# Performance work log

Hardware: AMD Instinct MI355X
Metric: run time of the kernel (lower is better)

Reference implementation:

```python
import jax, jax.numpy as jnp
import numpy as np

B, L, D = 4, 2048, 768
H, K = 12, 9
IPG = D // H  # in-channels per group = head_size = 64
PAD = (K - 1) // 2


def setup_inputs() -> dict:
    key = jax.random.key(0)
    ks = jax.random.split(key, 8)
    s = lambda k, shape, scale: jax.random.normal(k, shape, dtype=jnp.float32) * scale
    return {
        "query": s(ks[0], (B, L, D), 1.0),
        "dw_w": s(ks[1], (D, 1, K), 0.1),          # depthwise Conv1d weight, no bias
        "pw_w": s(ks[2], (H, IPG, IPG), 0.05),     # grouped 1x1 conv [head, out_pg, in_pg]
        "pw_b": s(ks[3], (D,), 0.02),
        "ak_w": s(ks[4], (H, K, IPG), 0.05),       # conv_attn_kernel grouped 1x1 [head, K, in_pg]
        "ak_b": s(ks[5], (H * K,), 0.02),
        "pt_w": s(ks[6], (D, D), 0.02),            # conv_attn_point Linear weight [out, in]
        "pt_b": s(ks[7], (D,), 0.02),
    }


def _sdconv(query, dw_w, pw_w, pw_b, ak_w, ak_b, pt_w, pt_b):
    b, l, d = query.shape
    # SeparableConv1d: depthwise conv (groups=D, kernel K, padding PAD, no bias)
    x = query.transpose(0, 2, 1)  # [B, D, L]
    dw = jax.lax.conv_general_dilated(
        x, dw_w, window_strides=(1,), padding=[(PAD, PAD)],
        feature_group_count=d, dimension_numbers=("NCH", "OIH", "NCH"))  # [B, D, L]
    # grouped pointwise conv (groups=H, kernel 1)
    dwg = dw.reshape(b, H, IPG, l)
    pw = jnp.einsum("bhil,hoi->bhol", dwg, pw_w).reshape(b, d, l) + pw_b[None, :, None]
    key_conv_attn = pw.transpose(0, 2, 1)  # [B, L, D]
    # stride == 1 path: elementwise gate with query
    conv_attn = key_conv_attn * query  # [B, L, D]
    # conv_attn_kernel: grouped 1x1 conv D -> H*K (per head: IPG -> K)
    ca = conv_attn.reshape(b, l, H, IPG)
    kern = jnp.einsum("blhi,hki->blhk", ca, ak_w) + ak_b.reshape(H, K)  # [B, L, H, K]
    w = jax.nn.softmax(kern, axis=-1)  # softmax over kernel positions
    # conv_attn_point linear on value (= query here)
    v = query @ pt_w.T + pt_b  # [B, L, D]
    # unfold: local windows of size K around each position
    vp = jnp.pad(v, ((0, 0), (PAD, PAD), (0, 0)))
    idx = jnp.arange(l)[:, None] + jnp.arange(K)[None, :]  # [L, K]
    win = vp[:, idx]  # [B, L, K, D]
    winh = win.reshape(b, l, K, H, IPG)
    out = jnp.einsum("blkhd,blhk->blhd", winh, w).reshape(b, l, d)
    return out


def reference(query, dw_w, pw_w, pw_b, ak_w, ak_b, pt_w, pt_b):
    return _sdconv(query, dw_w, pw_w, pw_b, ak_w, ak_b, pt_w, pt_b)
```

## Files before the change

kernel.cpp:

```cpp
#include <hip/hip_runtime.h>
#include <math.h>

#define NB 4
#define NL 2048
#define ND 768
#define NH 12
#define NK 9
#define NIPG 64
#define NPAD 4
#define LT 16
#define NGEMM 768

typedef __attribute__((ext_vector_type(8))) short s16x8;
typedef __attribute__((ext_vector_type(4))) float f32x4;

__device__ __forceinline__ unsigned short f2bf(float f) {
  unsigned int u = __float_as_uint(f);
  unsigned int r = (u + 0x7FFFu + ((u >> 16) & 1u)) >> 16;
  return (unsigned short)r;
}
__device__ __forceinline__ float bf2f(unsigned short s) {
  return __uint_as_float(((unsigned int)s) << 16);
}
__device__ __forceinline__ void gload16(const void* g, void* l) {
  __builtin_amdgcn_global_load_lds((const __attribute__((address_space(1))) void*)g,
                                   (__attribute__((address_space(3))) void*)l,
                                   16, 0, 0);
}

__global__ __launch_bounds__(256) void prep(const float* __restrict__ q,
                                            const float* __restrict__ pt_w,
                                            const float* __restrict__ pw_w,
                                            const float* __restrict__ ak_w,
                                            unsigned short* __restrict__ qb,
                                            unsigned short* __restrict__ ptb,
                                            unsigned short* __restrict__ pwb,
                                            unsigned short* __restrict__ akp) {
  const int t = blockIdx.x * 256 + threadIdx.x;
  for (int i = t; i < NB * NL * ND / 4; i += gridDim.x * 256) {
    float4 f = ((const float4*)q)[i];
    ushort4 o; o.x = f2bf(f.x); o.y = f2bf(f.y); o.z = f2bf(f.z); o.w = f2bf(f.w);
    ((ushort4*)qb)[i] = o;
  }
  if (t < ND * ND / 4) {
    float4 f = ((const float4*)pt_w)[t];
    ushort4 o; o.x = f2bf(f.x); o.y = f2bf(f.y); o.z = f2bf(f.z); o.w = f2bf(f.w);
    ((ushort4*)ptb)[t] = o;
  }
  if (t < NH * NIPG * NIPG / 4) {
    float4 f = ((const float4*)pw_w)[t];
    ushort4 o; o.x = f2bf(f.x); o.y = f2bf(f.y); o.z = f2bf(f.z); o.w = f2bf(f.w);
    ((ushort4*)pwb)[t] = o;
  }
  if (t < NH * 16 * NIPG) {
    const int h = t >> 10;
    const int r = t & 1023;
    const int k = r >> 6;
    const int i = r & 63;
    akp[t] = (k < NK) ? f2bf(ak_w[((size_t)h * NK + k) * NIPG + i]) : (unsigned short)0;
  }
}

__global__ __launch_bounds__(256) void fused(const unsigned short* __restrict__ qb,
                                             const unsigned short* __restrict__ ptb,
                                             const float* __restrict__ bias,
                                             unsigned short* __restrict__ v,
                                             const float* __restrict__ dw_w,
                                             const unsigned short* __restrict__ pwb,
                                             const float* __restrict__ pw_b,
                                             const unsigned short* __restrict__ akp,
                                             const float* __restrict__ ak_b,
                                             float* __restrict__ wout) {
  __shared__ unsigned char smem[24576];
  const int t = threadIdx.x;
  const int lane = t & 63;
  const int wv = t >> 6;
  const int fr = lane & 15;
  const int fq = lane >> 4;

  if (blockIdx.x < NGEMM) {
    const int g = blockIdx.x;
    const int xcd = g & 7;
    const int j = g >> 3;
    const long mo = (long)(xcd * 8 + j / 12) * 128;
    const int n0 = (j % 12) * 64;

    const int soff = t * 16;
    const int sr = soff >> 6;
    const int scb = soff & 63;
    const unsigned char* gA0 = (const unsigned char*)qb + (mo + sr) * 1536L + scb;
    const unsigned char* gA1 = gA0 + 64L * 1536;
    const unsigned char* gB  = (const unsigned char*)ptb + (size_t)(n0 + sr) * 1536 + scb;

    int aoff[2], boff[4];
#pragma unroll
    for (int m = 0; m < 2; ++m)
      aoff[m] = ((wv * 32 + m * 16 + fr) * 32 + fq * 8) * 2;
#pragma unroll
    for (int n = 0; n < 4; ++n)
      boff[n] = 8192 + ((n * 16 + fr) * 32 + fq * 8) * 2;

#define STAGE(kt_)                                                 \
    do {                                                           \
      const long kb_ = (long)(kt_) * 64;                           \
      unsigned char* base_ = &smem[((kt_) & 1) * 12288];           \
      gload16(gA0 + kb_, base_ + soff);                            \
      gload16(gA1 + kb_, base_ + 4096 + soff);                     \
      gload16(gB + kb_, base_ + 8192 + soff);                      \
    } while (0)

#define FRAGS(kt_)                                                 \
    do {                                                           \
      const unsigned char* bb_ = &smem[((kt_) & 1) * 12288];       \
      _Pragma("unroll")                                            \
      for (int m_ = 0; m_ < 2; ++m_) av[m_] = *(const s16x8*)&bb_[aoff[m_]]; \
      _Pragma("unroll")                                            \
      for (int n_ = 0; n_ < 4; ++n_) bv[n_] = *(const s16x8*)&bb_[boff[n_]]; \
    } while (0)

#define MM8                                                        \
    do {                                                           \
      _Pragma("unroll")                                            \
      for (int m_ = 0; m_ < 2; ++m_)                               \
        _Pragma("unroll")                                          \
        for (int n_ = 0; n_ < 4; ++n_)                             \
          acc[m_][n_] = __builtin_amdgcn_mfma_f32_16x16x32_bf16(   \
              av[m_], bv[n_], acc[m_][n_], 0, 0, 0);               \
    } while (0)

    f32x4 acc[2][4] = {};
    s16x8 av[2], bv[4];

    STAGE(0);
    STAGE(1);
    for (int kt = 0; kt < 23; ++kt) {
      asm volatile("s_waitcnt vmcnt(3)" ::: "memory");
      __builtin_amdgcn_s_barrier();
      FRAGS(kt);
      asm volatile("s_waitcnt lgkmcnt(0)" ::: "memory");
      __builtin_amdgcn_sched_barrier(0);
      __builtin_amdgcn_s_barrier();
      if (kt + 2 < 24) STAGE(kt + 2);
      MM8;
    }
    {
      asm volatile("s_waitcnt vmcnt(0)" ::: "memory");
      __builtin_amdgcn_s_barrier();
      FRAGS(23);
      MM8;
    }
#undef STAGE
#undef FRAGS
#undef MM8

#pragma unroll
    for (int m = 0; m < 2; ++m) {
#pragma unroll
      for (int n = 0; n < 4; ++n) {
        const long row = mo + wv * 32 + m * 16 + fq * 4;
        const int col = n0 + n * 16 + fr;
        const float bbv = bias[col];
#pragma unroll
        for (int jj = 0; jj < 4; ++jj)
          v[(row + jj) * ND + col] = f2bf(acc[m][n][jj] + bbv);
      }
    }
  } else {
    const int a = blockIdx.x - NGEMM;
    const int l0 = (a & 31) * 64;
    const int h  = (a >> 5) % NH;
    const int b  = a / (32 * NH);
    const int d0 = h * NIPG;

    unsigned short (*qs)[68] = (unsigned short(*)[68])smem;
    unsigned char* ab = smem + 9792;

    const unsigned short* pwh = pwb + (size_t)h * NIPG * NIPG;
    const unsigned short* akh = akp + (size_t)h * 16 * NIPG;
    s16x8 pv0[4], pv1[4];
#pragma unroll
    for (int n = 0; n < 4; ++n) {
      const int o = n * 16 + fr;
      pv0[n] = *(const s16x8*)&pwh[o * 64 + fq * 8];
      pv1[n] = *(const s16x8*)&pwh[o * 64 + 32 + fq * 8];
    }
    s16x8 ak0 = *(const s16x8*)&akh[fr * 64 + fq * 8];
    s16x8 ak1 = *(const s16x8*)&akh[fr * 64 + 32 + fq * 8];
    float dwk[NK];
#pragma unroll
    for (int k = 0; k < NK; ++k) dwk[k] = dw_w[(size_t)(d0 + lane) * NK + k];

    {
      const int sl = t >> 4;
      const int sc = (t & 15) * 4;
      for (int r = sl; r < 72; r += 16) {
        const int l = l0 - NPAD + r;
        ushort4 ub = make_ushort4(0, 0, 0, 0);
        if (l >= 0 && l < NL)
          ub = *(const ushort4*)&qb[((size_t)(b * NL + l)) * ND + d0 + sc];
        *(ushort4*)&qs[r][sc] = ub;
      }
    }
    __syncthreads();

    const int lset = wv * 16;
    {
      float win9[NK];
#pragma unroll
      for (int k = 0; k < NK; ++k) win9[k] = bf2f(qs[lset + k][lane]);
#pragma unroll
      for (int l2 = 0; l2 < 16; ++l2) {
        const int l = lset + l2;
        float s = 0.f;
#pragma unroll
        for (int k = 0; k < NK; ++k) s = fmaf(win9[k], dwk[k], s);
        const int byte = ((l * 64 + lane) * 2) ^ ((l & 7) << 4);
        *(unsigned short*)&ab[byte] = f2bf(s);
        if (l2 < 15) {
#pragma unroll
          for (int k = 0; k < NK - 1; ++k) win9[k] = win9[k + 1];
          win9[NK - 1] = bf2f(qs[lset + l2 + NK][lane]);
        }
      }
    }

    s16x8 av0, av1;
    {
      const int row = lset + fr;
      const int b0 = ((row * 64 + fq * 8) * 2)      ^ ((row & 7) << 4);
      const int b1 = ((row * 64 + 32 + fq * 8) * 2) ^ ((row & 7) << 4);
      av0 = *(const s16x8*)&ab[b0];
      av1 = *(const s16x8*)&ab[b1];
    }
    f32x4 accp[4];
#pragma unroll
    for (int n = 0; n < 4; ++n) {
      accp[n] = (f32x4){0.f, 0.f, 0.f, 0.f};
      accp[n] = __builtin_amdgcn_mfma_f32_16x16x32_bf16(av0, pv0[n], accp[n], 0, 0, 0);
      accp[n] = __builtin_amdgcn_mfma_f32_16x16x32_bf16(av1, pv1[n], accp[n], 0, 0, 0);
    }

#pragma unroll
    for (int n = 0; n < 4; ++n) {
      const int o = n * 16 + fr;
      const float pb = pw_b[d0 + o];
#pragma unroll
      for (int jj = 0; jj < 4; ++jj) {
        const int row = lset + fq * 4 + jj;
        const float ca = (accp[n][jj] + pb) * bf2f(qs[row + NPAD][o]);
        const int byte = ((row * 64 + o) * 2) ^ ((row & 7) << 4);
        *(unsigned short*)&ab[byte] = f2bf(ca);
      }
    }

    f32x4 acck = (f32x4){0.f, 0.f, 0.f, 0.f};
    {
      const int row = lset + fr;
      const int b0 = ((row * 64 + fq * 8) * 2)      ^ ((row & 7) << 4);
      const int b1 = ((row * 64 + 32 + fq * 8) * 2) ^ ((row & 7) << 4);
      s16x8 a0 = *(const s16x8*)&ab[b0];
      s16x8 a1 = *(const s16x8*)&ab[b1];
      acck = __builtin_amdgcn_mfma_f32_16x16x32_bf16(a0, ak0, acck, 0, 0, 0);
      acck = __builtin_amdgcn_mfma_f32_16x16x32_bf16(a1, ak1, acck, 0, 0, 0);
    }

    const bool kvalid = fr < NK;
    const float akbv = kvalid ? ak_b[h * NK + fr] : 0.f;
#pragma unroll
    for (int jj = 0; jj < 4; ++jj) {
      float val = acck[jj] + akbv;
      float mv = kvalid ? val : -3.4e38f;
#pragma unroll
      for (int mm = 1; mm < 16; mm <<= 1) mv = fmaxf(mv, __shfl_xor(mv, mm));
      const float e = kvalid ? __expf(val - mv) : 0.f;
      float ssum = e;
#pragma unroll
      for (int mm = 1; mm < 16; mm <<= 1) ssum += __shfl_xor(ssum, mm);
      if (kvalid) {
        const int row = l0 + lset + fq * 4 + jj;
        wout[(((size_t)(b * NL + row)) * NH + h) * NK + fr] = e / ssum;
      }
    }
  }
}

__global__ __launch_bounds__(192) void sdconv_out(const unsigned short* __restrict__ v,
                                                  const float* __restrict__ w,
                                                  float* __restrict__ out) {
  const int b  = blockIdx.y;
  const int l0 = blockIdx.x * LT;
  const int t  = threadIdx.x;
  const int d  = t * 4;
  const int h  = t >> 4;
  const size_t vbase = (size_t)b * NL * ND + d;

  float4 win[NK];
#pragma unroll
  for (int k = 0; k < NK; ++k) {
    const int r = l0 - NPAD + k;
    if (r >= 0 && r < NL) {
      ushort4 u = *(const ushort4*)&v[vbase + (size_t)r * ND];
      win[k] = make_float4(bf2f(u.x), bf2f(u.y), bf2f(u.z), bf2f(u.w));
    } else {
      win[k] = make_float4(0.f, 0.f, 0.f, 0.f);
    }
  }
#pragma unroll
  for (int l2 = 0; l2 < LT; ++l2) {
    const int l = l0 + l2;
    const float* wp = &w[(((size_t)(b * NL + l)) * NH + h) * NK];
    float4 acc = make_float4(0.f, 0.f, 0.f, 0.f);
#pragma unroll
    for (int k = 0; k < NK; ++k) {
      const float wk = wp[k];
      acc.x = fmaf(wk, win[k].x, acc.x);
      acc.y = fmaf(wk, win[k].y, acc.y);
      acc.z = fmaf(wk, win[k].z, acc.z);
      acc.w = fmaf(wk, win[k].w, acc.w);
    }
    *(float4*)&out[(size_t)(b * NL + l) * ND + d] = acc;
#pragma unroll
    for (int k = 0; k < NK - 1; ++k) win[k] = win[k + 1];
    const int rn = l + NPAD + 1;
    if (rn < NL) {
      ushort4 u = *(const ushort4*)&v[vbase + (size_t)rn * ND];
      win[NK - 1] = make_float4(bf2f(u.x), bf2f(u.y), bf2f(u.z), bf2f(u.w));
    } else {
      win[NK - 1] = make_float4(0.f, 0.f, 0.f, 0.f);
    }
  }
}

extern "C" void kernel_launch(void* const* d_in, const int* in_sizes, int n_in,
                              void* d_out, int out_size, void* d_ws, size_t ws_size,
                              hipStream_t stream) {
  const float* query = (const float*)d_in[0];
  const float* dw_w  = (const float*)d_in[1];
  const float* pw_w  = (const float*)d_in[2];
  const float* pw_b  = (const float*)d_in[3];
  const float* ak_w  = (const float*)d_in[4];
  const float* ak_b  = (const float*)d_in[5];
  const float* pt_w  = (const float*)d_in[6];
  const float* pt_b  = (const float*)d_in[7];
  float* out = (float*)d_out;

  float* w = (float*)d_ws;
  unsigned short* qb  = (unsigned short*)(w + (size_t)NB * NL * NH * NK);
  unsigned short* ptb = qb + (size_t)NB * NL * ND;
  unsigned short* pwb = ptb + (size_t)ND * ND;
  unsigned short* akp = pwb + (size_t)NH * NIPG * NIPG;
  unsigned short* v   = akp + (size_t)NH * 16 * NIPG;

  prep<<<2048, 256, 0, stream>>>(query, pt_w, pw_w, ak_w, qb, ptb, pwb, akp);

  fused<<<NGEMM + 32 * NH * NB, 256, 0, stream>>>(qb, ptb, pt_b, v,
                                                  dw_w, pwb, pw_b, akp, ak_b, w);

  dim3 g3(NL / LT, NB, 1);
  sdconv_out<<<g3, 192, 0, stream>>>(v, w, out);
}
```

Baseline: 138.6 us.

## Enlarge GEMM tiles to 128x128 and process two tiles per attention block

The projection GEMM moves from 128x64 to 128x128 output tiles with a 2x2 wave layout, so each wave computes 64x64 and fetched fragments get more reuse. This halves the GEMM block count and raises LDS use to 32KB. The attention-weight branch now handles two consecutive 64-row tiles per block, amortising the per-block weight loads, at the cost of an extra barrier and half as many blocks. Together these cut total blocks and redundant loads but raise register pressure and may lower occupancy.

```diff
diff --git a/kernel.cpp b/kernel.cpp
--- a/kernel.cpp
+++ b/kernel.cpp
@@ -9,7 +9,7 @@
 #define NIPG 64
 #define NPAD 4
 #define LT 16
-#define NGEMM 768
+#define NGEMM 384
 
 typedef __attribute__((ext_vector_type(8))) short s16x8;
 typedef __attribute__((ext_vector_type(4))) float f32x4;
@@ -71,7 +71,7 @@
                                              const unsigned short* __restrict__ akp,
                                              const float* __restrict__ ak_b,
                                              float* __restrict__ wout) {
-  __shared__ unsigned char smem[24576];
+  __shared__ unsigned char smem[32768];
   const int t = threadIdx.x;
   const int lane = t & 63;
   const int wv = t >> 6;
@@ -82,83 +82,86 @@
     const int g = blockIdx.x;
     const int xcd = g & 7;
     const int j = g >> 3;
-    const long mo = (long)(xcd * 8 + j / 12) * 128;
-    const int n0 = (j % 12) * 64;
+    const long mo = (long)(xcd * 8 + j / 6) * 128;
+    const int n0 = (j % 6) * 128;
+    const int wr = wv >> 1, wc = wv & 1;
 
     const int soff = t * 16;
     const int sr = soff >> 6;
     const int scb = soff & 63;
     const unsigned char* gA0 = (const unsigned char*)qb + (mo + sr) * 1536L + scb;
     const unsigned char* gA1 = gA0 + 64L * 1536;
-    const unsigned char* gB  = (const unsigned char*)ptb + (size_t)(n0 + sr) * 1536 + scb;
-
-    int aoff[2], boff[4];
-#pragma unroll
-    for (int m = 0; m < 2; ++m)
-      aoff[m] = ((wv * 32 + m * 16 + fr) * 32 + fq * 8) * 2;
+    const unsigned char* gB0 = (const unsigned char*)ptb + (size_t)(n0 + sr) * 1536 + scb;
+    const unsigned char* gB1 = gB0 + 64L * 1536;
+
+    int aoff[4], boff[4];
+#pragma unroll
+    for (int m = 0; m < 4; ++m)
+      aoff[m] = ((wr * 64 + m * 16 + fr) * 32 + fq * 8) * 2;
 #pragma unroll
     for (int n = 0; n < 4; ++n)
-      boff[n] = 8192 + ((n * 16 + fr) * 32 + fq * 8) * 2;
+      boff[n] = 8192 + ((wc * 64 + n * 16 + fr) * 32 + fq * 8) * 2;
 
 #define STAGE(kt_)                                                 \
     do {                                                           \
       const long kb_ = (long)(kt_) * 64;                           \
-      unsigned char* base_ = &smem[((kt_) & 1) * 12288];           \
+      unsigned char* base_ = &smem[((kt_) & 1) * 16384];           \
       gload16(gA0 + kb_, base_ + soff);                            \
       gload16(gA1 + kb_, base_ + 4096 + soff);                     \
-      gload16(gB + kb_, base_ + 8192 + soff);                      \
+      gload16(gB0 + kb_, base_ + 8192 + soff);                     \
+      gload16(gB1 + kb_, base_ + 12288 + soff);                    \
     } while (0)
 
 #define FRAGS(kt_)                                                 \
     do {                                                           \
-      const unsigned char* bb_ = &smem[((kt_) & 1) * 12288];       \
+      const unsigned char* bb_ = &smem[((kt_) & 1) * 16384];       \
       _Pragma("unroll")                                            \
-      for (int m_ = 0; m_ < 2; ++m_) av[m_] = *(const s16x8*)&bb_[aoff[m_]]; \
+      for (int m_ = 0; m_ < 4; ++m_) av[m_] = *(const s16x8*)&bb_[aoff[m_]]; \
       _Pragma("unroll")                                            \
       for (int n_ = 0; n_ < 4; ++n_) bv[n_] = *(const s16x8*)&bb_[boff[n_]]; \
     } while (0)
 
-#define MM8                                                        \
+#define MM16                                                       \
     do {                                                           \
       _Pragma("unroll")                                            \
-      for (int m_ = 0; m_ < 2; ++m_)                               \
+      for (int m_ = 0; m_ < 4; ++m_)                               \
         _Pragma("unroll")                                          \
         for (int n_ = 0; n_ < 4; ++n_)                             \
           acc[m_][n_] = __builtin_amdgcn_mfma_f32_16x16x32_bf16(   \
               av[m_], bv[n_], acc[m_][n_], 0, 0, 0);               \
     } while (0)
 
-    f32x4 acc[2][4] = {};
-    s16x8 av[2], bv[4];
+    f32x4 acc[4][4] = {};
+    s16x8 av[4], bv[4];
 
     STAGE(0);
     STAGE(1);
     for (int kt = 0; kt < 23; ++kt) {
-      asm volatile("s_waitcnt vmcnt(3)" ::: "memory");
+      asm volatile("s_waitcnt vmcnt(4)" ::: "memory");
       __builtin_amdgcn_s_barrier();
       FRAGS(kt);
       asm volatile("s_waitcnt lgkmcnt(0)" ::: "memory");
       __builtin_amdgcn_sched_barrier(0);
       __builtin_amdgcn_s_barrier();
       if (kt + 2 < 24) STAGE(kt + 2);
-      MM8;
+      MM16;
     }
     {
       asm volatile("s_waitcnt vmcnt(0)" ::: "memory");
       __builtin_amdgcn_s_barrier();
       FRAGS(23);
-      MM8;
+      MM16;
     }
 #undef STAGE
 #undef FRAGS
-#undef MM8
-
-#pragma unroll
-    for (int m = 0; m < 2; ++m) {
+#undef MM16
+
+#pragma unroll
+    for (int m = 0; m < 4; ++m) {
 #pragma unroll
       for (int n = 0; n < 4; ++n) {
-        const long row = mo + wv * 32 + m * 16 + fq * 4;
-        const int col = n0 + n * 16 + fr;
+        const long row = mo + wr * 64 + m * 16 + fq * 4;
+        const int col = n0 + wc * 64 + n * 16 + fr;
         const float bbv = bias[col];
 #pragma unroll
         for (int jj = 0; jj < 4; ++jj)
@@ -166,10 +169,10 @@
       }
     }
   } else {
-    const int a = blockIdx.x - NGEMM;
-    const int l0 = (a & 31) * 64;
-    const int h  = (a >> 5) % NH;
-    const int b  = a / (32 * NH);
+    const int a2 = blockIdx.x - NGEMM;
+    const int idx0 = a2 * 2;
+    const int h  = (idx0 >> 5) % NH;
+    const int b  = idx0 / (32 * NH);
     const int d0 = h * NIPG;
 
     unsigned short (*qs)[68] = (unsigned short(*)[68])smem;
@@ -189,96 +192,101 @@
     float dwk[NK];
 #pragma unroll
     for (int k = 0; k < NK; ++k) dwk[k] = dw_w[(size_t)(d0 + lane) * NK + k];
-
-    {
-      const int sl = t >> 4;
-      const int sc = (t & 15) * 4;
-      for (int r = sl; r < 72; r += 16) {
-        const int l = l0 - NPAD + r;
-        ushort4 ub = make_ushort4(0, 0, 0, 0);
-        if (l >= 0 && l < NL)
-          ub = *(const ushort4*)&qb[((size_t)(b * NL + l)) * ND + d0 + sc];
-        *(ushort4*)&qs[r][sc] = ub;
-      }
-    }
-    __syncthreads();
-
-    const int lset = wv * 16;
-    {
-      float win9[NK];
-#pragma unroll
-      for (int k = 0; k < NK; ++k) win9[k] = bf2f(qs[lset + k][lane]);
-#pragma unroll
-      for (int l2 = 0; l2 < 16; ++l2) {
-        const int l = lset + l2;
-        float s = 0.f;
-#pragma unroll
-        for (int k = 0; k < NK; ++k) s = fmaf(win9[k], dwk[k], s);
-        const int byte = ((l * 64 + lane) * 2) ^ ((l & 7) << 4);
-        *(unsigned short*)&ab[byte] = f2bf(s);
-        if (l2 < 15) {
-#pragma unroll
-          for (int k = 0; k < NK - 1; ++k) win9[k] = win9[k + 1];
-          win9[NK - 1] = bf2f(qs[lset + l2 + NK][lane]);
-        }
-      }
-    }
-
-    s16x8 av0, av1;
-    {
-      const int row = lset + fr;
-      const int b0 = ((row * 64 + fq * 8) * 2)      ^ ((row & 7) << 4);
-      const int b1 = ((row * 64 + 32 + fq * 8) * 2) ^ ((row & 7) << 4);
-      av0 = *(const s16x8*)&ab[b0];
-      av1 = *(const s16x8*)&ab[b1];
-    }
-    f32x4 accp[4];
-#pragma unroll
-    for (int n = 0; n < 4; ++n) {
-      accp[n] = (f32x4){0.f, 0.f, 0.f, 0.f};
-      accp[n] = __builtin_amdgcn_mfma_f32_16x16x32_bf16(av0, pv0[n], accp[n], 0, 0, 0);
-      accp[n] = __builtin_amdgcn_mfma_f32_16x16x32_bf16(av1, pv1[n], accp[n], 0, 0, 0);
-    }
-
-#pragma unroll
-    for (int n = 0; n < 4; ++n) {
-      const int o = n * 16 + fr;
-      const float pb = pw_b[d0 + o];
-#pragma unroll
-      for (int jj = 0; jj < 4; ++jj) {
-        const int row = lset + fq * 4 + jj;
-        const float ca = (accp[n][jj] + pb) * bf2f(qs[row + NPAD][o]);
-        const int byte = ((row * 64 + o) * 2) ^ ((row & 7) << 4);
-        *(unsigned short*)&ab[byte] = f2bf(ca);
-      }
-    }
-
-    f32x4 acck = (f32x4){0.f, 0.f, 0.f, 0.f};
-    {
-      const int row = lset + fr;
-      const int b0 = ((row * 64 + fq * 8) * 2)      ^ ((row & 7) << 4);
-      const int b1 = ((row * 64 + 32 + fq * 8) * 2) ^ ((row & 7) << 4);
-      s16x8 a0 = *(const s16x8*)&ab[b0];
-      s16x8 a1 = *(const s16x8*)&ab[b1];
-      acck = __builtin_amdgcn_mfma_f32_16x16x32_bf16(a0, ak0, acck, 0, 0, 0);
-      acck = __builtin_amdgcn_mfma_f32_16x16x32_bf16(a1, ak1, acck, 0, 0, 0);
-    }
-
     const bool kvalid = fr < NK;
     const float akbv = kvalid ? ak_b[h * NK + fr] : 0.f;
-#pragma unroll
-    for (int jj = 0; jj < 4; ++jj) {
-      float val = acck[jj] + akbv;
-      float mv = kvalid ? val : -3.4e38f;
-#pragma unroll
-      for (int mm = 1; mm < 16; mm <<= 1) mv = fmaxf(mv, __shfl_xor(mv, mm));
-      const float e = kvalid ? __expf(val - mv) : 0.f;
-      float ssum = e;
-#pragma unroll
-      for (int mm = 1; mm < 16; mm <<= 1) ssum += __shfl_xor(ssum, mm);
-      if (kvalid) {
-        const int row = l0 + lset + fq * 4 + jj;
-        wout[(((size_t)(b * NL + row)) * NH + h) * NK + fr] = e / ssum;
+    const int lset = wv * 16;
+
+    for (int u = 0; u < 2; ++u) {
+      const int l0 = ((idx0 + u) & 31) * 64;
+      if (u > 0) __syncthreads();
+
+      {
+        const int sl = t >> 4;
+        const int sc = (t & 15) * 4;
+        for (int r = sl; r < 72; r += 16) {
+          const int l = l0 - NPAD + r;
+          ushort4 ub = make_ushort4(0, 0, 0, 0);
+          if (l >= 0 && l < NL)
+            ub = *(const ushort4*)&qb[((size_t)(b * NL + l)) * ND + d0 + sc];
+          *(ushort4*)&qs[r][sc] = ub;
+        }
+      }
+      __syncthreads();
+
+      {
+        float win9[NK];
+#pragma unroll
+        for (int k = 0; k < NK; ++k) win9[k] = bf2f(qs[lset + k][lane]);
+#pragma unroll
+        for (int l2 = 0; l2 < 16; ++l2) {
+          const int l = lset + l2;
+          float s = 0.f;
+#pragma unroll
+          for (int k = 0; k < NK; ++k) s = fmaf(win9[k], dwk[k], s);
+          const int byte = ((l * 64 + lane) * 2) ^ ((l & 7) << 4);
+          *(unsigned short*)&ab[byte] = f2bf(s);
+          if (l2 < 15) {
+#pragma unroll
+            for (int k = 0; k < NK - 1; ++k) win9[k] = win9[k + 1];
+            win9[NK - 1] = bf2f(qs[lset + l2 + NK][lane]);
+          }
+        }
+      }
+
+      s16x8 av0, av1;
+      {
+        const int row = lset + fr;
+        const int b0 = ((row * 64 + fq * 8) * 2)      ^ ((row & 7) << 4);
+        const int b1 = ((row * 64 + 32 + fq * 8) * 2) ^ ((row & 7) << 4);
+        av0 = *(const s16x8*)&ab[b0];
+        av1 = *(const s16x8*)&ab[b1];
+      }
+      f32x4 accp[4];
+#pragma unroll
+      for (int n = 0; n < 4; ++n) {
+        accp[n] = (f32x4){0.f, 0.f, 0.f, 0.f};
+        accp[n] = __builtin_amdgcn_mfma_f32_16x16x32_bf16(av0, pv0[n], accp[n], 0, 0, 0);
+        accp[n] = __builtin_amdgcn_mfma_f32_16x16x32_bf16(av1, pv1[n], accp[n], 0, 0, 0);
+      }
+
+#pragma unroll
+      for (int n = 0; n < 4; ++n) {
+        const int o = n * 16 + fr;
+        const float pb = pw_b[d0 + o];
+#pragma unroll
+        for (int jj = 0; jj < 4; ++jj) {
+          const int row = lset + fq * 4 + jj;
+          const float ca = (accp[n][jj] + pb) * bf2f(qs[row + NPAD][o]);
+          const int byte = ((row * 64 + o) * 2) ^ ((row & 7) << 4);
+          *(unsigned short*)&ab[byte] = f2bf(ca);
+        }
+      }
+
+      f32x4 acck = (f32x4){0.f, 0.f, 0.f, 0.f};
+      {
+        const int row = lset + fr;
+        const int b0 = ((row * 64 + fq * 8) * 2)      ^ ((row & 7) << 4);
+        const int b1 = ((row * 64 + 32 + fq * 8) * 2) ^ ((row & 7) << 4);
+        s16x8 a0 = *(const s16x8*)&ab[b0];
+        s16x8 a1 = *(const s16x8*)&ab[b1];
+        acck = __builtin_amdgcn_mfma_f32_16x16x32_bf16(a0, ak0, acck, 0, 0, 0);
+        acck = __builtin_amdgcn_mfma_f32_16x16x32_bf16(a1, ak1, acck, 0, 0, 0);
+      }
+
+#pragma unroll
+      for (int jj = 0; jj < 4; ++jj) {
+        float val = acck[jj] + akbv;
+        float mv = kvalid ? val : -3.4e38f;
+#pragma unroll
+        for (int mm = 1; mm < 16; mm <<= 1) mv = fmaxf(mv, __shfl_xor(mv, mm));
+        const float e = kvalid ? __expf(val - mv) : 0.f;
+        float ssum = e;
+#pragma unroll
+        for (int mm = 1; mm < 16; mm <<= 1) ssum += __shfl_xor(ssum, mm);
+        if (kvalid) {
+          const int row = l0 + lset + fq * 4 + jj;
+          wout[(((size_t)(b * NL + row)) * NH + h) * NK + fr] = e / ssum;
+        }
       }
     }
   }
@@ -353,8 +361,8 @@
 
   prep<<<2048, 256, 0, stream>>>(query, pt_w, pw_w, ak_w, qb, ptb, pwb, akp);
 
-  fused<<<NGEMM + 32 * NH * NB, 256, 0, stream>>>(qb, ptb, pt_b, v,
-                                                  dw_w, pwb, pw_b, akp, ak_b, w);
+  fused<<<NGEMM + 32 * NH * NB / 2, 256, 0, stream>>>(qb, ptb, pt_b, v,
+                                                      dw_w, pwb, pw_b, akp, ak_b, w);
 
   dim3 g3(NL / LT, NB, 1);
   sdconv_out<<<g3, 192, 0, stream>>>(v, w, out);
```

Measured after the change: 140.4 us. Within noise of the previous version (+1.3%).
